# Kernel optimization log

Measured on AMD Instinct MI355X. Metric: run time of the kernel, lower is better.

The kernel has to match this reference:

```python
import jax, jax.numpy as jnp
import numpy as np
from jax import lax

B, T, S_ENC = 64, 32, 64
E, H, V = 1024, 1024, 32000


def setup_inputs() -> dict:
    key = jax.random.key(0)
    ks = jax.random.split(key, 12)
    s = 0.02
    return {
        "inputs": jax.random.randint(ks[0], (B, T), 0, V),
        "encoder_outputs": jax.random.normal(ks[1], (B, S_ENC, 2 * H), jnp.float32),
        "h0": jax.random.normal(ks[2], (B, H), jnp.float32) * 0.1,
        "c0": jax.random.normal(ks[3], (B, H), jnp.float32) * 0.1,
        "emb": jax.random.normal(ks[4], (V, E), jnp.float32) * s,
        "W_ih": jax.random.normal(ks[5], (4 * H, E), jnp.float32) * s,
        "W_hh": jax.random.normal(ks[6], (4 * H, H), jnp.float32) * s,
        "b_ih": jnp.zeros((4 * H,), jnp.float32),
        "b_hh": jnp.zeros((4 * H,), jnp.float32),
        "attn_W": jax.random.normal(ks[7], (2 * H, H), jnp.float32) * s,  # Linear(H -> 2H, no bias)
        "comb_W": jax.random.normal(ks[8], (H, 3 * H), jnp.float32) * s,  # Linear(3H -> H)
        "comb_b": jnp.zeros((H,), jnp.float32),
        "out_W": jax.random.normal(ks[9], (V, H), jnp.float32) * s,       # Linear(H -> V)
        "out_b": jnp.zeros((V,), jnp.float32),
    }


def _decode(inputs, encoder_outputs, h0, c0, emb, W_ih, W_hh, b_ih, b_hh,
            attn_W, comb_W, comb_b, out_W, out_b):
    x = emb[inputs]                      # [B, T, E]
    bias = b_ih + b_hh

    def step(carry, x_t):
        h, c = carry                     # [B, H] each
        gates = x_t @ W_ih.T + h @ W_hh.T + bias    # [B, 4H]
        i, f, g, o = jnp.split(gates, 4, axis=-1)   # PyTorch LSTM gate order
        i, f, o = jax.nn.sigmoid(i), jax.nn.sigmoid(f), jax.nn.sigmoid(o)
        c = f * c + i * jnp.tanh(g)
        h = o * jnp.tanh(c)
        # Luong-style attention (faithful to source, incl. softmax over dim=1 of size 1)
        ah = h @ attn_W.T                                        # [B, 2H]
        scores = jnp.einsum('bd,bsd->bs', ah, encoder_outputs)[:, None, :]  # [B,1,S]
        w = jax.nn.softmax(scores, axis=1)                       # size-1 axis -> all ones
        ctx = jnp.einsum('bqs,bsd->bqd', w, encoder_outputs)[:, 0]          # [B, 2H]
        merged = jnp.concatenate([h, ctx], axis=-1)              # [B, 3H]
        out = jnp.tanh(merged @ comb_W.T + comb_b)               # [B, H]
        return (h, c), out

    (h, c), outs = lax.scan(step, (h0, c0), x.transpose(1, 0, 2))
    outputs = outs.transpose(1, 0, 2)                            # [B, T, H]
    logits = outputs @ out_W.T + out_b                           # [B, T, V]
    return logits, h, c


def reference(inputs, encoder_outputs, h0, c0, emb, W_ih, W_hh, b_ih, b_hh,
              attn_W, comb_W, comb_b, out_W, out_b):
    return _decode(inputs, encoder_outputs, h0, c0, emb, W_ih, W_hh, b_ih, b_hh,
                   attn_W, comb_W, comb_b, out_W, out_b)
```

## Files before the change

kernel.cpp:

```cpp
#include <hip/hip_runtime.h>
#include <hip/hip_bf16.h>


typedef unsigned short u16;
typedef unsigned int u32;
typedef short s8v __attribute__((ext_vector_type(8)));
typedef float f4v __attribute__((ext_vector_type(4)));

__device__ __forceinline__ u16 f2bf(float f) {
  unsigned x = __float_as_uint(f);
  return (u16)((x + 0x7fffu + ((x >> 16) & 1u)) >> 16);
}
__device__ __forceinline__ float bf2f(u16 u) {
  return __uint_as_float(((unsigned)u) << 16);
}

__device__ __forceinline__ void gl_lds16(const void* g, void* l) {
  __builtin_amdgcn_global_load_lds(
      (const __attribute__((address_space(1))) u32*)g,
      (__attribute__((address_space(3))) u32*)l, 16, 0, 0);
}

__device__ __forceinline__ int xcd_swz(int bid, int nb) {
  int q8 = nb >> 3, r8 = nb & 7;
  int xcd = bid & 7, idx = bid >> 3;
  return (xcd < r8 ? xcd * (q8 + 1) : r8 * (q8 + 1) + (xcd - r8) * q8) + idx;
}

template <int EPI>
__global__ __launch_bounds__(512, 1) void gemm_r(
    const u16* __restrict__ A, const u16* __restrict__ Bm,
    const float* __restrict__ bias, void* __restrict__ Cp,
    int K, int ldc, int gridM) {
  __shared__ __align__(16) u16 LDS[4 * 16384];

  int swz = xcd_swz((int)blockIdx.x, (int)gridDim.x);
  int mt = swz % gridM, nt = swz / gridM;
  long bm = (long)mt * 256, bn = (long)nt * 256;

  int tid = threadIdx.x;
  int w = tid >> 6, l = tid & 63;
  int wm = w & 1, wn = w >> 1;
  int lr = l & 15, lg = l >> 4;

  int nt_k = K >> 5;

  auto stage = [&](int s, int kt_idx) {
    int kt = kt_idx << 5;
    u16* sa = &LDS[s * 16384];
    u16* sb = &LDS[s * 16384 + 8192];
#pragma unroll
    for (int ch = 0; ch < 2; ++ch) {
      int cb = ch * 512 + w * 64;
      int c = cb + l;
      int row = c >> 2, sp = c & 3;
      int sl = sp ^ ((row >> 1) & 3);
      gl_lds16(A + (bm + row) * (long)K + kt + sl * 8, sa + cb * 8);
      gl_lds16(Bm + (bn + row) * (long)K + kt + sl * 8, sb + cb * 8);
    }
  };

  f4v acc[8][4];
#pragma unroll
  for (int i = 0; i < 8; ++i)
#pragma unroll
    for (int j = 0; j < 4; ++j) acc[i][j] = (f4v){0.f, 0.f, 0.f, 0.f};

  stage(0, 0);
  if (1 < nt_k) stage(1, 1);
  if (2 < nt_k) stage(2, 2);
  asm volatile("s_waitcnt vmcnt(8)" ::: "memory");
  __builtin_amdgcn_s_barrier();
  __builtin_amdgcn_sched_barrier(0);

  for (int t = 0; t < nt_k; ++t) {
    if (t + 3 < nt_k) stage((t + 3) & 3, t + 3);
    const u16* sa = &LDS[(t & 3) * 16384];
    const u16* sb = &LDS[(t & 3) * 16384 + 8192];
    s8v av[8], bv[4];
#pragma unroll
    for (int i = 0; i < 8; ++i) {
      int ra = wm * 128 + i * 16 + lr;
      int pa = lg ^ ((ra >> 1) & 3);
      av[i] = *(const s8v*)((const char*)sa + ra * 64 + pa * 16);
    }
#pragma unroll
    for (int i = 0; i < 4; ++i) {
      int rb = wn * 64 + i * 16 + lr;
      int pb = lg ^ ((rb >> 1) & 3);
      bv[i] = *(const s8v*)((const char*)sb + rb * 64 + pb * 16);
    }
    __builtin_amdgcn_s_setprio(1);
#pragma unroll
    for (int mi = 0; mi < 8; ++mi)
#pragma unroll
      for (int ni = 0; ni < 4; ++ni)
        acc[mi][ni] = __builtin_amdgcn_mfma_f32_16x16x32_bf16(
            av[mi], bv[ni], acc[mi][ni], 0, 0, 0);
    __builtin_amdgcn_s_setprio(0);
    if (t + 1 >= nt_k) break;
    if (t + 3 < nt_k) {
      asm volatile("s_waitcnt vmcnt(8)" ::: "memory");
    } else if (t + 2 < nt_k) {
      asm volatile("s_waitcnt vmcnt(4)" ::: "memory");
    } else {
      asm volatile("s_waitcnt vmcnt(0)" ::: "memory");
    }
    __builtin_amdgcn_s_barrier();
    __builtin_amdgcn_sched_barrier(0);
  }

#pragma unroll
  for (int mi = 0; mi < 8; ++mi) {
#pragma unroll
    for (int q = 0; q < 4; ++q) {
      long row = bm + wm * 128 + mi * 16 + lg * 4 + q;
#pragma unroll
      for (int ni = 0; ni < 4; ++ni) {
        long col = bn + wn * 64 + ni * 16 + lr;
        float v = acc[mi][ni][q] + bias[col];
        if (EPI == 3)
          ((float*)Cp)[row * (long)ldc + col] = v;
        else
          ((u16*)Cp)[row * (long)ldc + col] = f2bf(v);
      }
    }
  }
}

template <int EPI, int PERM>
__global__ __launch_bounds__(512, 1) void gemm_p(
    const u16* __restrict__ A, const u16* __restrict__ Bm,
    const float* __restrict__ bias, void* __restrict__ Cp,
    int K, int ldc, int gridM) {
  __shared__ __align__(16) u16 LDS[3 * 24576];

  int swz = xcd_swz((int)blockIdx.x, (int)gridDim.x);
  int mt = swz % gridM, nt = swz / gridM;
  long bm = (long)mt * 128, bn = (long)nt * 256;

  int tid = threadIdx.x;
  int w = tid >> 6, l = tid & 63;
  int wm = w & 1, wn = w >> 1;
  int lr = l & 15, lg = l >> 4;

  int nt_k = K >> 6;

  auto stage = [&](int s, int kt_idx) {
    int kt = kt_idx << 6;
    u16* sa = &LDS[s * 24576];
    u16* sb = &LDS[s * 24576 + 8192];
#pragma unroll
    for (int ch = 0; ch < 2; ++ch) {
      int cb = ch * 512 + w * 64;
      int c = cb + l;
      int row = c >> 3, sp = c & 7;
      gl_lds16(A + (bm + row) * (long)K + kt + ((sp ^ (row & 7)) << 3),
               sa + cb * 8);
    }
#pragma unroll
    for (int ch = 0; ch < 4; ++ch) {
      int cb = ch * 512 + w * 64;
      int c = cb + l;
      int row = c >> 3, sp = c & 7;
      gl_lds16(Bm + (bn + row) * (long)K + kt + ((sp ^ (row & 7)) << 3),
               sb + cb * 8);
    }
  };

  f4v acc[4][4];
#pragma unroll
  for (int i = 0; i < 4; ++i)
#pragma unroll
    for (int j = 0; j < 4; ++j) acc[i][j] = (f4v){0.f, 0.f, 0.f, 0.f};

  stage(0, 0);
  stage(1, 1);
  asm volatile("s_waitcnt vmcnt(6)" ::: "memory");
  __builtin_amdgcn_s_barrier();
  __builtin_amdgcn_sched_barrier(0);

  for (int t = 0; t < nt_k; ++t) {
    if (t + 2 < nt_k) stage((t + 2) % 3, t + 2);
    const u16* sa = &LDS[(t % 3) * 24576];
    const u16* sb = &LDS[(t % 3) * 24576 + 8192];
#pragma unroll
    for (int ks = 0; ks < 2; ++ks) {
      s8v av[4], bv[4];
#pragma unroll
      for (int i = 0; i < 4; ++i) {
        int ra = wm * 64 + i * 16 + lr;
        int pa = (ks * 4 + lg) ^ (ra & 7);
        av[i] = *(const s8v*)((const char*)sa + ra * 128 + pa * 16);
        int rb = wn * 64 + i * 16 + lr;
        int pb = (ks * 4 + lg) ^ (rb & 7);
        bv[i] = *(const s8v*)((const char*)sb + rb * 128 + pb * 16);
      }
      __builtin_amdgcn_s_setprio(1);
#pragma unroll
      for (int mi = 0; mi < 4; ++mi)
#pragma unroll
        for (int ni = 0; ni < 4; ++ni)
          acc[mi][ni] = __builtin_amdgcn_mfma_f32_16x16x32_bf16(
              av[mi], bv[ni], acc[mi][ni], 0, 0, 0);
      __builtin_amdgcn_s_setprio(0);
    }
    if (t + 1 >= nt_k) break;
    if (t + 2 < nt_k) {
      asm volatile("s_waitcnt vmcnt(6)" ::: "memory");
    } else {
      asm volatile("s_waitcnt vmcnt(0)" ::: "memory");
    }
    __builtin_amdgcn_s_barrier();
    __builtin_amdgcn_sched_barrier(0);
  }

#pragma unroll
  for (int mi = 0; mi < 4; ++mi) {
#pragma unroll
    for (int q = 0; q < 4; ++q) {
      long row = bm + wm * 64 + mi * 16 + lg * 4 + q;
#pragma unroll
      for (int ni = 0; ni < 4; ++ni) {
        long col = bn + wn * 64 + ni * 16 + lr;
        float v = acc[mi][ni][q] + bias[col];
        if (PERM) {
          long prow = (row & 31) * 64 + (row >> 5);
          long pcol = (col & 1023) * 4 + (col >> 10);
          ((u16*)Cp)[prow * 4096 + pcol] = f2bf(v);
        } else if (EPI == 3) {
          ((float*)Cp)[row * (long)ldc + col] = v;
        } else {
          ((u16*)Cp)[row * (long)ldc + col] = f2bf(v);
        }
      }
    }
  }
}

template <int EPI>
__global__ __launch_bounds__(256, 2) void gemm_bt2(
    const u16* __restrict__ A, const u16* __restrict__ Bm,
    const float* __restrict__ bias, void* __restrict__ Cp,
    int K, int ldc, int gridM) {
  __shared__ __align__(16) u16 As[128 * 64];
  __shared__ __align__(16) u16 Bs[128 * 64];

  int swz = xcd_swz((int)blockIdx.x, (int)gridDim.x);
  int mt = swz % gridM, nt = swz / gridM;
  long bm = (long)mt * 128, bn = (long)nt * 128;

  int tid = threadIdx.x;
  int w = tid >> 6, l = tid & 63;
  int wm = (w & 1) * 64, wn = (w >> 1) * 64;
  int lr = l & 15, lg = l >> 4;

  f4v acc[4][4];
#pragma unroll
  for (int i = 0; i < 4; ++i)
#pragma unroll
    for (int j = 0; j < 4; ++j) acc[i][j] = (f4v){0.f, 0.f, 0.f, 0.f};

  for (int kt = 0; kt < K; kt += 64) {
#pragma unroll
    for (int p = 0; p < 4; ++p) {
      int cb = (p * 4 + w) * 64;
      int c = cb + l;
      int row = c >> 3, ce = (c & 7) * 8;
      gl_lds16(A + (bm + row) * (long)K + kt + ce, &As[cb * 8]);
      gl_lds16(Bm + (bn + row) * (long)K + kt + ce, &Bs[cb * 8]);
    }
    __syncthreads();
#pragma unroll
    for (int ks = 0; ks < 2; ++ks) {
      int kb = ks * 64 + lg * 16;
      s8v av[4], bv[4];
#pragma unroll
      for (int i = 0; i < 4; ++i) {
        av[i] = *(const s8v*)((const char*)&As[0] + (wm + i * 16 + lr) * 128 + kb);
        bv[i] = *(const s8v*)((const char*)&Bs[0] + (wn + i * 16 + lr) * 128 + kb);
      }
#pragma unroll
      for (int mi = 0; mi < 4; ++mi)
#pragma unroll
        for (int ni = 0; ni < 4; ++ni)
          acc[mi][ni] = __builtin_amdgcn_mfma_f32_16x16x32_bf16(
              av[mi], bv[ni], acc[mi][ni], 0, 0, 0);
    }
    __syncthreads();
  }
#pragma unroll
  for (int mi = 0; mi < 4; ++mi) {
#pragma unroll
    for (int q = 0; q < 4; ++q) {
      long row = bm + wm + mi * 16 + lg * 4 + q;
#pragma unroll
      for (int ni = 0; ni < 4; ++ni) {
        long col = bn + wn + ni * 16 + lr;
        float v = acc[mi][ni][q] + bias[col];
        if (EPI == 2) v = tanhf(v);
        if (EPI == 3)
          ((float*)Cp)[row * (long)ldc + col] = v;
        else
          ((u16*)Cp)[row * (long)ldc + col] = f2bf(v);
      }
    }
  }
}

template <int EPI, int PERM>
__global__ __launch_bounds__(256, 2) void gemm_btf(
    const u16* __restrict__ A, const float* __restrict__ Bm,
    const float* __restrict__ bias, void* __restrict__ Cp,
    int K, int ldc, int gridM) {
  __shared__ __align__(16) u16 As[128][72];
  __shared__ __align__(16) u16 Bs[128][72];
  int swz = xcd_swz((int)blockIdx.x, (int)gridDim.x);
  int mt = swz % gridM, nt = swz / gridM;
  long bm = (long)mt * 128, bn = (long)nt * 128;
  int tid = threadIdx.x;
  int w = tid >> 6, l = tid & 63;
  int wm = (w & 1) * 64, wn = (w >> 1) * 64;
  int lr = l & 15, lg = l >> 4;
  f4v acc[4][4];
#pragma unroll
  for (int i = 0; i < 4; ++i)
#pragma unroll
    for (int j = 0; j < 4; ++j) acc[i][j] = (f4v){0.f, 0.f, 0.f, 0.f};
  for (int kt = 0; kt < K; kt += 64) {
#pragma unroll
    for (int p = 0; p < 4; ++p) {
      int ch = p * 256 + tid;
      int row = ch >> 3, cc = ch & 7;
      *(uint4*)((char*)(&As[0][0]) + row * 144 + cc * 16) =
          *(const uint4*)(A + (bm + row) * (long)K + kt + cc * 8);
      const float* bp = Bm + (bn + row) * (long)K + kt + cc * 8;
      float4 b0 = *(const float4*)bp;
      float4 b1 = *(const float4*)(bp + 4);
      union { u16 t8[8]; uint4 v; } cv;
      cv.t8[0] = f2bf(b0.x); cv.t8[1] = f2bf(b0.y);
      cv.t8[2] = f2bf(b0.z); cv.t8[3] = f2bf(b0.w);
      cv.t8[4] = f2bf(b1.x); cv.t8[5] = f2bf(b1.y);
      cv.t8[6] = f2bf(b1.z); cv.t8[7] = f2bf(b1.w);
      *(uint4*)((char*)(&Bs[0][0]) + row * 144 + cc * 16) = cv.v;
    }
    __syncthreads();
#pragma unroll
    for (int ks = 0; ks < 2; ++ks) {
      int kb = ks * 64 + lg * 16;
      s8v av[4], bv[4];
#pragma unroll
      for (int i = 0; i < 4; ++i) {
        av[i] = *(const s8v*)((const char*)(&As[0][0]) + (wm + i * 16 + lr) * 144 + kb);
        bv[i] = *(const s8v*)((const char*)(&Bs[0][0]) + (wn + i * 16 + lr) * 144 + kb);
      }
#pragma unroll
      for (int mi = 0; mi < 4; ++mi)
#pragma unroll
        for (int ni = 0; ni < 4; ++ni)
          acc[mi][ni] = __builtin_amdgcn_mfma_f32_16x16x32_bf16(
              av[mi], bv[ni], acc[mi][ni], 0, 0, 0);
    }
    __syncthreads();
  }
#pragma unroll
  for (int mi = 0; mi < 4; ++mi) {
#pragma unroll
    for (int q = 0; q < 4; ++q) {
      long row = bm + wm + mi * 16 + lg * 4 + q;
#pragma unroll
      for (int ni = 0; ni < 4; ++ni) {
        long col = bn + wn + ni * 16 + lr;
        float v = acc[mi][ni][q] + bias[col];
        if (EPI == 2) v = tanhf(v);
        if (PERM) {
          long prow = (row & 31) * 64 + (row >> 5);
          long pcol = (col & 1023) * 4 + (col >> 10);
          ((u16*)Cp)[prow * 4096 + pcol] = f2bf(v);
        } else if (EPI == 3) {
          ((float*)Cp)[row * (long)ldc + col] = v;
        } else {
          ((u16*)Cp)[row * (long)ldc + col] = f2bf(v);
        }
      }
    }
  }
}

__global__ __launch_bounds__(256, 1) void lstm_step3(
    const u16* __restrict__ Whh, const u16* __restrict__ xprojT,
    const u16* __restrict__ h_in, u16* __restrict__ h_next,
    float* __restrict__ c_buf, u16* __restrict__ a2,
    float* __restrict__ hf, float* __restrict__ cf, int t) {
  __shared__ __align__(16) u16 Hs[32 * 1024];
  __shared__ __align__(16) u16 Ws[32 * 1024];
  __shared__ float Gs[32][33];

  int bid = blockIdx.x;
  int j = bid & 127, bh = bid >> 7;
  int colbase = j * 8;
  int tid = threadIdx.x, w = tid >> 6, l = tid & 63;
  int bq = w & 1, nh = w >> 1;
  int lr = l & 15, lg = l >> 4;

  int hi = tid >> 7;
  int ps = tid & 127;
#pragma unroll
  for (int p = 0; p < 16; ++p) {
    int r = 2 * p + hi;
    int sl = ps ^ (r & 7);
    gl_lds16(h_in + (bh * 32 + r) * 1024 + sl * 8, &Hs[(p * 4 + w) * 512]);
    int g = r >> 3, rr = r & 7;
    gl_lds16(Whh + (long)(g * 1024 + colbase + rr) * 1024 + sl * 8,
             &Ws[(p * 4 + w) * 512]);
  }

  int eb = tid >> 3, er = tid & 7;
  int gb = bh * 32 + eb, ecol = colbase + er;
  uint2 xv = *(const uint2*)(xprojT + ((long)t * 64 + gb) * 4096 + ecol * 4);
  float co = c_buf[gb * 1024 + ecol];
  __syncthreads();

  int ar = bq * 16 + lr;
  int br = nh * 16 + lr;
  int axor = (ar & 7), bxor = (br & 7);
  f4v acc0 = {0.f, 0.f, 0.f, 0.f}, acc1 = {0.f, 0.f, 0.f, 0.f};
#pragma unroll
  for (int kc = 0; kc < 32; kc += 2) {
    {
      int s = kc * 4 + lg;
      s8v av = *(const s8v*)((const char*)Hs + ar * 2048 + (s ^ axor) * 16);
      s8v bv = *(const s8v*)((const char*)Ws + br * 2048 + (s ^ bxor) * 16);
      acc0 = __builtin_amdgcn_mfma_f32_16x16x32_bf16(av, bv, acc0, 0, 0, 0);
    }
    {
      int s = (kc + 1) * 4 + lg;
      s8v av = *(const s8v*)((const char*)Hs + ar * 2048 + (s ^ axor) * 16);
      s8v bv = *(const s8v*)((const char*)Ws + br * 2048 + (s ^ bxor) * 16);
      acc1 = __builtin_amdgcn_mfma_f32_16x16x32_bf16(av, bv, acc1, 0, 0, 0);
    }
  }
#pragma unroll
  for (int q = 0; q < 4; ++q)
    Gs[bq * 16 + lg * 4 + q][nh * 16 + lr] = acc0[q] + acc1[q];
  __syncthreads();

  float pi = Gs[eb][er]      + bf2f((u16)(xv.x));
  float pf = Gs[eb][8 + er]  + bf2f((u16)(xv.x >> 16));
  float pg = Gs[eb][16 + er] + bf2f((u16)(xv.y));
  float po = Gs[eb][24 + er] + bf2f((u16)(xv.y >> 16));
  float iv = 1.f / (1.f + expf(-pi));
  float fv = 1.f / (1.f + expf(-pf));
  float ov = 1.f / (1.f + expf(-po));
  float gv = tanhf(pg);
  float cn = fv * co + iv * gv;
  float hn = ov * tanhf(cn);
  c_buf[gb * 1024 + ecol] = cn;
  u16 hb = f2bf(hn);
  h_next[gb * 1024 + ecol] = hb;
  a2[(long)(gb * 32 + t) * 3072 + ecol] = hb;
  if (t == 31) {
    hf[gb * 1024 + ecol] = hn;
    cf[gb * 1024 + ecol] = cn;
  }
}

__global__ void k_misc(const float* __restrict__ bih, const float* __restrict__ bhh,
                       const float* __restrict__ h0, const float* __restrict__ c0,
                       float* __restrict__ bias, u16* __restrict__ hbuf0,
                       float* __restrict__ cbuf) {
  int i = blockIdx.x * 256 + threadIdx.x;
  if (i < 4096) bias[i] = bih[i] + bhh[i];
  if (i < 65536) {
    hbuf0[i] = f2bf(h0[i]);
    cbuf[i] = c0[i];
  }
}

__global__ void k_cvt8(const float* __restrict__ src, u16* __restrict__ dst, int n8) {
  int i = blockIdx.x * 256 + threadIdx.x;
  if (i >= n8) return;
  const float4* s = (const float4*)(src + (long)i * 8);
  float4 a = s[0], b = s[1];
  union { u16 t[8]; uint4 v; } cv;
  cv.t[0] = f2bf(a.x); cv.t[1] = f2bf(a.y); cv.t[2] = f2bf(a.z); cv.t[3] = f2bf(a.w);
  cv.t[4] = f2bf(b.x); cv.t[5] = f2bf(b.y); cv.t[6] = f2bf(b.z); cv.t[7] = f2bf(b.w);
  ((uint4*)dst)[i] = cv.v;
}

__global__ void k_emb8(const int* __restrict__ inp, const float* __restrict__ emb,
                       u16* __restrict__ dst) {
  int i = blockIdx.x * 256 + threadIdx.x;
  int r = i >> 7, k8 = (i & 127) * 8;
  const float* s = emb + (long)inp[r] * 1024 + k8;
  float4 a = *(const float4*)s, b = *(const float4*)(s + 4);
  union { u16 t[8]; uint4 v; } cv;
  cv.t[0] = f2bf(a.x); cv.t[1] = f2bf(a.y); cv.t[2] = f2bf(a.z); cv.t[3] = f2bf(a.w);
  cv.t[4] = f2bf(b.x); cv.t[5] = f2bf(b.y); cv.t[6] = f2bf(b.z); cv.t[7] = f2bf(b.w);
  ((uint4*)dst)[i] = cv.v;
}

__global__ void k_ctx2(const float* __restrict__ enc, u16* __restrict__ a2) {
  int b = blockIdx.x;
  int dg = threadIdx.x;
  float s[8] = {0.f, 0.f, 0.f, 0.f, 0.f, 0.f, 0.f, 0.f};
  for (int si = 0; si < 64; ++si) {
    const float* p = enc + ((long)(b * 64 + si)) * 2048 + dg * 8;
    float4 x = *(const float4*)p, y = *(const float4*)(p + 4);
    s[0] += x.x; s[1] += x.y; s[2] += x.z; s[3] += x.w;
    s[4] += y.x; s[5] += y.y; s[6] += y.z; s[7] += y.w;
  }
  union { u16 t[8]; uint4 v; } cv;
#pragma unroll
  for (int e = 0; e < 8; ++e) cv.t[e] = f2bf(s[e]);
  for (int t = 0; t < 32; ++t)
    *(uint4*)(a2 + (long)(b * 32 + t) * 3072 + 1024 + dg * 8) = cv.v;
}

extern "C" void kernel_launch(void* const* d_in, const int* in_sizes, int n_in,
                              void* d_out, int out_size, void* d_ws, size_t ws_size,
                              hipStream_t stream) {
  (void)in_sizes; (void)n_in; (void)out_size;
  const int*   inputs = (const int*)d_in[0];
  const float* enc    = (const float*)d_in[1];
  const float* h0     = (const float*)d_in[2];
  const float* c0     = (const float*)d_in[3];
  const float* emb    = (const float*)d_in[4];
  const float* Wih    = (const float*)d_in[5];
  const float* Whh    = (const float*)d_in[6];
  const float* bih    = (const float*)d_in[7];
  const float* bhh    = (const float*)d_in[8];
  const float* combW  = (const float*)d_in[10];
  const float* combb  = (const float*)d_in[11];
  const float* outW   = (const float*)d_in[12];
  const float* outb   = (const float*)d_in[13];
  float* out = (float*)d_out;

  char* ws = (char*)d_ws;
  size_t off = 0;
  auto alloc = [&](size_t bytes) {
    char* p = ws + off;
    off += (bytes + 255) & ~(size_t)255;
    return p;
  };
  u16*   WHH_BF = (u16*)  alloc(4096ull * 1024 * 2);
  u16*   XPROJ  = (u16*)  alloc(2048ull * 4096 * 2);
  u16*   EMBX   = (u16*)  alloc(2048ull * 1024 * 2);
  u16*   A2     = (u16*)  alloc(2048ull * 3072 * 2);
  u16*   OUTS   = (u16*)  alloc(2048ull * 1024 * 2);
  float* BIAS   = (float*)alloc(4096 * 4);
  u16*   HBUF   = (u16*)  alloc(2ull * 65536 * 2);
  float* CBUF   = (float*)alloc(65536 * 4);
  u16*   WIH_BF   = (u16*)alloc(4096ull * 1024 * 2);
  u16*   COMBW_BF = (u16*)alloc(1024ull * 3072 * 2);
  size_t off_w1 = off;
  u16*   OUTW_BF  = (u16*)alloc(32000ull * 1024 * 2);
  size_t off_w2 = off;
  bool haveW1 = ws_size >= off_w1;
  bool haveW2 = ws_size >= off_w2;

  k_misc<<<dim3(256), dim3(256), 0, stream>>>(bih, bhh, h0, c0, BIAS, HBUF, CBUF);
  k_cvt8<<<dim3(2048), dim3(256), 0, stream>>>(Whh, WHH_BF, 524288);
  k_emb8<<<dim3(1024), dim3(256), 0, stream>>>(inputs, emb, EMBX);
  k_ctx2<<<dim3(64), dim3(256), 0, stream>>>(enc, A2);
  if (haveW1) {
    k_cvt8<<<dim3(2048), dim3(256), 0, stream>>>(Wih, WIH_BF, 524288);
    k_cvt8<<<dim3(1536), dim3(256), 0, stream>>>(combW, COMBW_BF, 393216);
  }
  if (haveW2)
    k_cvt8<<<dim3(16000), dim3(256), 0, stream>>>(outW, OUTW_BF, 4096000);

  if (haveW1)
    gemm_p<1, 1><<<dim3(256), dim3(512), 0, stream>>>(EMBX, WIH_BF, BIAS, XPROJ,
                                                      1024, 4096, 16);
  else
    gemm_btf<1, 1><<<dim3(512), dim3(256), 0, stream>>>(EMBX, Wih, BIAS, XPROJ,
                                                        1024, 4096, 16);

  for (int t = 0; t < 32; ++t) {
    u16* hin  = HBUF + (t & 1) * 65536;
    u16* hout = HBUF + ((t + 1) & 1) * 65536;
    lstm_step3<<<dim3(256), dim3(256), 0, stream>>>(
        WHH_BF, XPROJ, hin, hout, CBUF, A2,
        out + 65536000, out + 65536000 + 65536, t);
  }

  if (haveW1)
    gemm_bt2<2><<<dim3(128), dim3(256), 0, stream>>>(A2, COMBW_BF, combb, OUTS,
                                                     3072, 1024, 16);
  else
    gemm_btf<2, 0><<<dim3(128), dim3(256), 0, stream>>>(A2, combW, combb, OUTS,
                                                        3072, 1024, 16);
  if (haveW2)
    gemm_r<3><<<dim3(1000), dim3(512), 0, stream>>>(OUTS, OUTW_BF, outb, d_out,
                                                    1024, 32000, 8);
  else
    gemm_btf<3, 0><<<dim3(4000), dim3(256), 0, stream>>>(OUTS, outW, outb, d_out,
                                                         1024, 32000, 16);
}
```

Baseline: 566.2 us.

## Use double-buffered BK=64 pipeline in output GEMM; load LSTM operands directly from global

The output-projection GEMM moves from a 4-stage, K=32 LDS pipeline to a 2-stage pipeline with K=64 tiles. The swizzle widens to 8 slots, and each stage is waited on with vmcnt(0). This halves the number of barriers per K sweep but gives up the deeper prefetch, so load latency may be exposed more. The per-timestep LSTM kernel drops its LDS staging of h and W_hh and reads MFMA operands straight from global memory with four independent accumulators. That removes the LDS round trip and one barrier, at the cost of uncoalesced global loads.

```diff
diff --git a/kernel.cpp b/kernel.cpp
--- a/kernel.cpp
+++ b/kernel.cpp
@@ -28,11 +28,11 @@
 }
 
 template <int EPI>
-__global__ __launch_bounds__(512, 1) void gemm_r(
+__global__ __launch_bounds__(512, 1) void gemm_q(
     const u16* __restrict__ A, const u16* __restrict__ Bm,
     const float* __restrict__ bias, void* __restrict__ Cp,
     int K, int ldc, int gridM) {
-  __shared__ __align__(16) u16 LDS[4 * 16384];
+  __shared__ __align__(16) u16 LDS[2 * 32768];
 
   int swz = xcd_swz((int)blockIdx.x, (int)gridDim.x);
   int mt = swz % gridM, nt = swz / gridM;
@@ -43,20 +43,20 @@
   int wm = w & 1, wn = w >> 1;
   int lr = l & 15, lg = l >> 4;
 
-  int nt_k = K >> 5;
+  int nt_k = K >> 6;
 
   auto stage = [&](int s, int kt_idx) {
-    int kt = kt_idx << 5;
-    u16* sa = &LDS[s * 16384];
-    u16* sb = &LDS[s * 16384 + 8192];
-#pragma unroll
-    for (int ch = 0; ch < 2; ++ch) {
+    int kt = kt_idx << 6;
+    u16* sa = &LDS[s * 32768];
+    u16* sb = &LDS[s * 32768 + 16384];
+#pragma unroll
+    for (int ch = 0; ch < 4; ++ch) {
       int cb = ch * 512 + w * 64;
       int c = cb + l;
-      int row = c >> 2, sp = c & 3;
-      int sl = sp ^ ((row >> 1) & 3);
-      gl_lds16(A + (bm + row) * (long)K + kt + sl * 8, sa + cb * 8);
-      gl_lds16(Bm + (bn + row) * (long)K + kt + sl * 8, sb + cb * 8);
+      int row = c >> 3, sp = c & 7;
+      int ko = kt + ((sp ^ (row & 7)) << 3);
+      gl_lds16(A + (bm + row) * (long)K + ko, sa + cb * 8);
+      gl_lds16(Bm + (bn + row) * (long)K + ko, sb + cb * 8);
     }
   };
 
@@ -67,45 +67,40 @@
     for (int j = 0; j < 4; ++j) acc[i][j] = (f4v){0.f, 0.f, 0.f, 0.f};
 
   stage(0, 0);
-  if (1 < nt_k) stage(1, 1);
-  if (2 < nt_k) stage(2, 2);
-  asm volatile("s_waitcnt vmcnt(8)" ::: "memory");
+  asm volatile("s_waitcnt vmcnt(0)" ::: "memory");
   __builtin_amdgcn_s_barrier();
   __builtin_amdgcn_sched_barrier(0);
 
   for (int t = 0; t < nt_k; ++t) {
-    if (t + 3 < nt_k) stage((t + 3) & 3, t + 3);
-    const u16* sa = &LDS[(t & 3) * 16384];
-    const u16* sb = &LDS[(t & 3) * 16384 + 8192];
-    s8v av[8], bv[4];
-#pragma unroll
-    for (int i = 0; i < 8; ++i) {
-      int ra = wm * 128 + i * 16 + lr;
-      int pa = lg ^ ((ra >> 1) & 3);
-      av[i] = *(const s8v*)((const char*)sa + ra * 64 + pa * 16);
-    }
-#pragma unroll
-    for (int i = 0; i < 4; ++i) {
-      int rb = wn * 64 + i * 16 + lr;
-      int pb = lg ^ ((rb >> 1) & 3);
-      bv[i] = *(const s8v*)((const char*)sb + rb * 64 + pb * 16);
-    }
-    __builtin_amdgcn_s_setprio(1);
-#pragma unroll
-    for (int mi = 0; mi < 8; ++mi)
-#pragma unroll
-      for (int ni = 0; ni < 4; ++ni)
-        acc[mi][ni] = __builtin_amdgcn_mfma_f32_16x16x32_bf16(
-            av[mi], bv[ni], acc[mi][ni], 0, 0, 0);
-    __builtin_amdgcn_s_setprio(0);
+    if (t + 1 < nt_k) stage((t + 1) & 1, t + 1);
+    const u16* sa = &LDS[(t & 1) * 32768];
+    const u16* sb = &LDS[(t & 1) * 32768 + 16384];
+#pragma unroll
+    for (int ks = 0; ks < 2; ++ks) {
+      s8v av[8], bv[4];
+#pragma unroll
+      for (int i = 0; i < 8; ++i) {
+        int ra = wm * 128 + i * 16 + lr;
+        int pa = (ks * 4 + lg) ^ (ra & 7);
+        av[i] = *(const s8v*)((const char*)sa + ra * 128 + pa * 16);
+      }
+#pragma unroll
+      for (int i = 0; i < 4; ++i) {
+        int rb = wn * 64 + i * 16 + lr;
+        int pb = (ks * 4 + lg) ^ (rb & 7);
+        bv[i] = *(const s8v*)((const char*)sb + rb * 128 + pb * 16);
+      }
+      __builtin_amdgcn_s_setprio(1);
+#pragma unroll
+      for (int mi = 0; mi < 8; ++mi)
+#pragma unroll
+        for (int ni = 0; ni < 4; ++ni)
+          acc[mi][ni] = __builtin_amdgcn_mfma_f32_16x16x32_bf16(
+              av[mi], bv[ni], acc[mi][ni], 0, 0, 0);
+      __builtin_amdgcn_s_setprio(0);
+    }
     if (t + 1 >= nt_k) break;
-    if (t + 3 < nt_k) {
-      asm volatile("s_waitcnt vmcnt(8)" ::: "memory");
-    } else if (t + 2 < nt_k) {
-      asm volatile("s_waitcnt vmcnt(4)" ::: "memory");
-    } else {
-      asm volatile("s_waitcnt vmcnt(0)" ::: "memory");
-    }
+    asm volatile("s_waitcnt vmcnt(0)" ::: "memory");
     __builtin_amdgcn_s_barrier();
     __builtin_amdgcn_sched_barrier(0);
   }
@@ -387,13 +382,11 @@
   }
 }
 
-__global__ __launch_bounds__(256, 1) void lstm_step3(
+__global__ __launch_bounds__(256, 1) void lstm_step4(
     const u16* __restrict__ Whh, const u16* __restrict__ xprojT,
     const u16* __restrict__ h_in, u16* __restrict__ h_next,
     float* __restrict__ c_buf, u16* __restrict__ a2,
     float* __restrict__ hf, float* __restrict__ cf, int t) {
-  __shared__ __align__(16) u16 Hs[32 * 1024];
-  __shared__ __align__(16) u16 Ws[32 * 1024];
   __shared__ float Gs[32][33];
 
   int bid = blockIdx.x;
@@ -403,46 +396,38 @@
   int bq = w & 1, nh = w >> 1;
   int lr = l & 15, lg = l >> 4;
 
-  int hi = tid >> 7;
-  int ps = tid & 127;
-#pragma unroll
-  for (int p = 0; p < 16; ++p) {
-    int r = 2 * p + hi;
-    int sl = ps ^ (r & 7);
-    gl_lds16(h_in + (bh * 32 + r) * 1024 + sl * 8, &Hs[(p * 4 + w) * 512]);
-    int g = r >> 3, rr = r & 7;
-    gl_lds16(Whh + (long)(g * 1024 + colbase + rr) * 1024 + sl * 8,
-             &Ws[(p * 4 + w) * 512]);
-  }
+  int ar = bq * 16 + lr;
+  int br = nh * 16 + lr;
+  const u16* arow = h_in + (bh * 32 + ar) * 1024 + lg * 8;
+  const u16* brow =
+      Whh + ((long)((br >> 3) * 1024 + colbase + (br & 7))) * 1024 + lg * 8;
 
   int eb = tid >> 3, er = tid & 7;
   int gb = bh * 32 + eb, ecol = colbase + er;
   uint2 xv = *(const uint2*)(xprojT + ((long)t * 64 + gb) * 4096 + ecol * 4);
   float co = c_buf[gb * 1024 + ecol];
-  __syncthreads();
-
-  int ar = bq * 16 + lr;
-  int br = nh * 16 + lr;
-  int axor = (ar & 7), bxor = (br & 7);
+
   f4v acc0 = {0.f, 0.f, 0.f, 0.f}, acc1 = {0.f, 0.f, 0.f, 0.f};
-#pragma unroll
-  for (int kc = 0; kc < 32; kc += 2) {
-    {
-      int s = kc * 4 + lg;
-      s8v av = *(const s8v*)((const char*)Hs + ar * 2048 + (s ^ axor) * 16);
-      s8v bv = *(const s8v*)((const char*)Ws + br * 2048 + (s ^ bxor) * 16);
-      acc0 = __builtin_amdgcn_mfma_f32_16x16x32_bf16(av, bv, acc0, 0, 0, 0);
-    }
-    {
-      int s = (kc + 1) * 4 + lg;
-      s8v av = *(const s8v*)((const char*)Hs + ar * 2048 + (s ^ axor) * 16);
-      s8v bv = *(const s8v*)((const char*)Ws + br * 2048 + (s ^ bxor) * 16);
-      acc1 = __builtin_amdgcn_mfma_f32_16x16x32_bf16(av, bv, acc1, 0, 0, 0);
-    }
+  f4v acc2 = {0.f, 0.f, 0.f, 0.f}, acc3 = {0.f, 0.f, 0.f, 0.f};
+#pragma unroll
+  for (int kc = 0; kc < 32; kc += 4) {
+    s8v a0 = *(const s8v*)(arow + (kc + 0) * 32);
+    s8v b0 = *(const s8v*)(brow + (kc + 0) * 32);
+    s8v a1 = *(const s8v*)(arow + (kc + 1) * 32);
+    s8v b1 = *(const s8v*)(brow + (kc + 1) * 32);
+    s8v a2r = *(const s8v*)(arow + (kc + 2) * 32);
+    s8v b2 = *(const s8v*)(brow + (kc + 2) * 32);
+    s8v a3 = *(const s8v*)(arow + (kc + 3) * 32);
+    s8v b3 = *(const s8v*)(brow + (kc + 3) * 32);
+    acc0 = __builtin_amdgcn_mfma_f32_16x16x32_bf16(a0, b0, acc0, 0, 0, 0);
+    acc1 = __builtin_amdgcn_mfma_f32_16x16x32_bf16(a1, b1, acc1, 0, 0, 0);
+    acc2 = __builtin_amdgcn_mfma_f32_16x16x32_bf16(a2r, b2, acc2, 0, 0, 0);
+    acc3 = __builtin_amdgcn_mfma_f32_16x16x32_bf16(a3, b3, acc3, 0, 0, 0);
   }
 #pragma unroll
   for (int q = 0; q < 4; ++q)
-    Gs[bq * 16 + lg * 4 + q][nh * 16 + lr] = acc0[q] + acc1[q];
+    Gs[bq * 16 + lg * 4 + q][nh * 16 + lr] =
+        acc0[q] + acc1[q] + acc2[q] + acc3[q];
   __syncthreads();
 
   float pi = Gs[eb][er]      + bf2f((u16)(xv.x));
@@ -580,7 +565,7 @@
   for (int t = 0; t < 32; ++t) {
     u16* hin  = HBUF + (t & 1) * 65536;
     u16* hout = HBUF + ((t + 1) & 1) * 65536;
-    lstm_step3<<<dim3(256), dim3(256), 0, stream>>>(
+    lstm_step4<<<dim3(256), dim3(256), 0, stream>>>(
         WHH_BF, XPROJ, hin, hout, CBUF, A2,
         out + 65536000, out + 65536000 + 65536, t);
   }
@@ -592,7 +577,7 @@
     gemm_btf<2, 0><<<dim3(128), dim3(256), 0, stream>>>(A2, combW, combb, OUTS,
                                                         3072, 1024, 16);
   if (haveW2)
-    gemm_r<3><<<dim3(1000), dim3(512), 0, stream>>>(OUTS, OUTW_BF, outb, d_out,
+    gemm_q<3><<<dim3(1000), dim3(512), 0, stream>>>(OUTS, OUTW_BF, outb, d_out,
                                                     1024, 32000, 8);
   else
     gemm_btf<3, 0><<<dim3(4000), dim3(256), 0, stream>>>(OUTS, outW, outb, d_out,
```

New measurement: 696.1 us. 1.23x slower.
